# Performance work log

Measured on AMD Instinct MI355X. Metric: run time of the kernel, lower is better.

Reference implementation:

```python
import jax, jax.numpy as jnp
import numpy as np

N = 30000      # nodes
E = 300000     # edges (before self-loops)
F_NODE = 32; F_EDGE = 16
HID = 64       # hidden_channels
H = 4; C = 64  # heads, per-head channels (GATConv out_channels = HID)
NEG_SLOPE_ATT = 0.2   # GATConv negative_slope
NEG_SLOPE_ACT = 0.01  # F.leaky_relu default
LN_EPS = 1e-5


def setup_inputs() -> dict:
    key = jax.random.key(0)
    ks = jax.random.split(key, 32)
    def w(k, shape, fan_in):
        return jax.random.normal(k, shape, jnp.float32) * (1.0 / np.sqrt(fan_in))
    inp = {
        "x": jax.random.normal(ks[0], (N, F_NODE), jnp.float32),
        "edge_index": jax.random.randint(ks[1], (2, E), 0, N),
        "edge_attr": jax.random.normal(ks[2], (E, F_EDGE), jnp.float32),
        "wn": w(ks[3], (F_NODE, HID), F_NODE), "bn": jnp.zeros((HID,), jnp.float32),
        "we": w(ks[4], (F_EDGE, HID), F_EDGE), "be": jnp.zeros((HID,), jnp.float32),
    }
    for i, off in ((1, 5), (2, 13)):
        inp[f"lin{i}"] = w(ks[off], (HID, H * C), HID)        # GATConv.lin
        inp[f"line{i}"] = w(ks[off + 1], (HID, H * C), HID)    # GATConv.lin_edge
        inp[f"as{i}"] = w(ks[off + 2], (H, C), C)              # att_src
        inp[f"ad{i}"] = w(ks[off + 3], (H, C), C)              # att_dst
        inp[f"ae{i}"] = w(ks[off + 4], (H, C), C)              # att_edge
        inp[f"b{i}"] = jnp.zeros((C,), jnp.float32)            # GATConv bias (concat=False -> C)
        inp[f"g{i}"] = jnp.ones((HID,), jnp.float32)           # LayerNorm weight
        inp[f"bt{i}"] = jnp.zeros((HID,), jnp.float32)         # LayerNorm bias
    return inp


def layernorm(x, g, b):
    mu = x.mean(-1, keepdims=True)
    v = ((x - mu) ** 2).mean(-1, keepdims=True)
    return (x - mu) / jnp.sqrt(v + LN_EPS) * g + b


def gat_layer(x, src, dst, e_attr, lin_w, lin_e_w, att_src, att_dst, att_edge, bias, n):
    # x: [n, HID]; e_attr: [E2, HID]; edge lists already include self-loops
    E2 = src.shape[0]
    h = (x @ lin_w).reshape(n, H, C)          # [n,H,C]
    e = (e_attr @ lin_e_w).reshape(E2, H, C)  # [E2,H,C]
    a_src = (h * att_src[None]).sum(-1)       # [n,H]
    a_dst = (h * att_dst[None]).sum(-1)       # [n,H]
    a_edge = (e * att_edge[None]).sum(-1)     # [E2,H]
    a = jax.nn.leaky_relu(a_src[src] + a_dst[dst] + a_edge, NEG_SLOPE_ATT)
    # scatter-softmax over destination neighborhoods (every node has a self-loop)
    m = jax.ops.segment_max(a, dst, num_segments=n)
    ex = jnp.exp(a - m[dst])
    den = jax.ops.segment_sum(ex, dst, num_segments=n)
    alpha = ex / den[dst]                     # [E2,H]
    out = jax.ops.segment_sum(h[src] * alpha[..., None], dst, num_segments=n)  # [n,H,C]
    return out.mean(axis=1) + bias, alpha     # concat=False: average heads


def reference(x, edge_index, edge_attr, wn, bn, we, be,
              lin1, line1, as1, ad1, ae1, b1, g1, bt1,
              lin2, line2, as2, ad2, ae2, b2, g2, bt2):
    n = x.shape[0]
    x = jax.nn.relu(x @ wn + bn)
    ea = jax.nn.relu(edge_attr @ we + be)
    src, dst = edge_index[0], edge_index[1]
    # PyG add_self_loops(fill_value='mean'): self-loop edge_attr = mean of incoming edge_attr
    ones = jnp.ones((src.shape[0],), ea.dtype)
    deg = jax.ops.segment_sum(ones, dst, num_segments=n)
    mean_ea = jax.ops.segment_sum(ea, dst, num_segments=n) / jnp.maximum(deg, 1.0)[:, None]
    loop = jnp.arange(n, dtype=src.dtype)
    src_f = jnp.concatenate([src, loop])
    dst_f = jnp.concatenate([dst, loop])
    ea_f = jnp.concatenate([ea, mean_ea], axis=0)
    h1, alpha1 = gat_layer(x, src_f, dst_f, ea_f, lin1, line1, as1, ad1, ae1, b1, n)
    h1 = layernorm(jax.nn.leaky_relu(h1, NEG_SLOPE_ACT), g1, bt1)
    # dropout is identity in eval mode
    h2, alpha2 = gat_layer(h1, src_f, dst_f, ea_f, lin2, line2, as2, ad2, ae2, b2, n)
    h2 = layernorm(jax.nn.leaky_relu(h2, NEG_SLOPE_ACT), g2, bt2)
    return h2, alpha1, alpha2
```

## Files before the change

### kernel.cpp

```cpp
#include <hip/hip_runtime.h>

#define FN 32
#define FE 16
#define HID 64
#define HEADS 4
#define CHC 64

__device__ __forceinline__ float bf2f(unsigned short u) {
  unsigned int x = ((unsigned int)u) << 16;
  return __builtin_bit_cast(float, x);
}
__device__ __forceinline__ unsigned short f2bf(float f) {
  unsigned int x = __builtin_bit_cast(unsigned int, f);
  unsigned int r = (x + 0x7fff + ((x >> 16) & 1)) >> 16;
  return (unsigned short)r;
}

__device__ __forceinline__ void reduce8_store(const float p[8],
    float* __restrict__ arr1, float* __restrict__ arr2, size_t pos, int lane)
{
  float q[4];
  {
    bool hi = lane & 1;
    #pragma unroll
    for (int m = 0; m < 4; m++) {
      float keep = hi ? p[m + 4] : p[m];
      float send = hi ? p[m] : p[m + 4];
      q[m] = keep + __shfl_xor(send, 1);
    }
  }
  float r[2];
  {
    bool hi = lane & 2;
    #pragma unroll
    for (int m = 0; m < 2; m++) {
      float keep = hi ? q[m + 2] : q[m];
      float send = hi ? q[m] : q[m + 2];
      r[m] = keep + __shfl_xor(send, 2);
    }
  }
  float s;
  {
    bool hi = lane & 4;
    float keep = hi ? r[1] : r[0];
    float send = hi ? r[0] : r[1];
    s = keep + __shfl_xor(send, 4);
  }
  s += __shfl_xor(s, 8);
  s += __shfl_xor(s, 16);
  s += __shfl_xor(s, 32);
  if (lane < 8) {
    int entry = ((lane & 1) << 2) | (lane & 2) | ((lane >> 2) & 1);
    if (entry < 4) arr1[pos * 4 + entry] = s;
    else           arr2[pos * 4 + entry - 4] = s;
  }
}

__global__ __launch_bounds__(256) void k_vecs(
    const float* __restrict__ lin1, const float* __restrict__ line1,
    const float* __restrict__ as1, const float* __restrict__ ad1,
    const float* __restrict__ ae1,
    const float* __restrict__ lin2, const float* __restrict__ line2,
    const float* __restrict__ as2, const float* __restrict__ ad2,
    const float* __restrict__ ae2,
    float* __restrict__ vS, float* __restrict__ vD, float* __restrict__ vE)
{
  int bi = blockIdx.x;
  int l = bi / 3, kind = bi % 3;
  const float* lin = (kind == 2) ? (l ? line2 : line1) : (l ? lin2 : lin1);
  const float* att = (kind == 0) ? (l ? as2 : as1)
                   : (kind == 1) ? (l ? ad2 : ad1) : (l ? ae2 : ae1);
  float* out = ((kind == 0) ? vS : (kind == 1) ? vD : vE) + l * 256;
  int t = threadIdx.x;
  int c = t >> 2, hd = t & 3;
  float acc = 0.f;
  for (int cc = 0; cc < CHC; cc++)
    acc += lin[c * (HEADS * CHC) + hd * CHC + cc] * att[hd * CHC + cc];
  out[c * 4 + hd] = acc;
}

__global__ __launch_bounds__(256) void k_x1(const float* __restrict__ x,
    const float* __restrict__ wn, const float* __restrict__ bn,
    const float* __restrict__ vS, const float* __restrict__ vD,
    float* __restrict__ x1, float* __restrict__ ssrc, float* __restrict__ sdst,
    int n)
{
  int t = threadIdx.x; int w = t >> 6; int lane = t & 63;
  int v = blockIdx.x * 4 + w;
  __shared__ float xs[4][FN];
  if (v < n && lane < FN) xs[w][lane] = x[(size_t)v * FN + lane];
  __syncthreads();
  if (v >= n) return;
  float acc = bn[lane];
  #pragma unroll
  for (int k = 0; k < FN; k++) acc += xs[w][k] * wn[k * HID + lane];
  acc = fmaxf(acc, 0.f);
  x1[(size_t)v * HID + lane] = acc;
  float4 s4 = ((const float4*)vS)[lane];
  float4 d4 = ((const float4*)vD)[lane];
  float p[8] = {acc * s4.x, acc * s4.y, acc * s4.z, acc * s4.w,
                acc * d4.x, acc * d4.y, acc * d4.z, acc * d4.w};
  reduce8_store(p, ssrc, sdst, (size_t)v, lane);
}

__global__ __launch_bounds__(256) void k_sdots(const float* __restrict__ xin,
    const float* __restrict__ vS, const float* __restrict__ vD,
    float* __restrict__ ssrc, float* __restrict__ sdst, int n)
{
  int t = threadIdx.x; int w = t >> 6; int lane = t & 63;
  int v = blockIdx.x * 4 + w;
  if (v >= n) return;
  float xc = xin[(size_t)v * HID + lane];
  float4 s4 = ((const float4*)vS)[lane];
  float4 d4 = ((const float4*)vD)[lane];
  float p[8] = {xc * s4.x, xc * s4.y, xc * s4.z, xc * s4.w,
                xc * d4.x, xc * d4.y, xc * d4.z, xc * d4.w};
  reduce8_store(p, ssrc, sdst, (size_t)v, lane);
}

__global__ __launch_bounds__(256) void k_deg(const int* __restrict__ dst,
                                             int* __restrict__ deg, int E)
{
  int e = blockIdx.x * 256 + threadIdx.x;
  if (e < E) atomicAdd(&deg[dst[e]], 1);
}

__global__ __launch_bounds__(1024) void k_scan1(const int* __restrict__ deg,
    int* __restrict__ rowptr, int* __restrict__ bsum, int n)
{
  __shared__ int wsum[16];
  int t = threadIdx.x, wv = t >> 6, lane = t & 63;
  int i = blockIdx.x * 1024 + t;
  int val = (i < n) ? deg[i] : 0;
  int sc = val;
  #pragma unroll
  for (int off = 1; off < 64; off <<= 1) {
    int u = __shfl_up(sc, off);
    if (lane >= off) sc += u;
  }
  if (lane == 63) wsum[wv] = sc;
  __syncthreads();
  int woff = 0;
  #pragma unroll
  for (int k = 0; k < 16; k++) woff += (k < wv) ? wsum[k] : 0;
  if (i < n) rowptr[i] = woff + sc - val;
  if (t == 0) {
    int tot = 0;
    #pragma unroll
    for (int k = 0; k < 16; k++) tot += wsum[k];
    bsum[blockIdx.x] = tot;
  }
}

__global__ __launch_bounds__(1024) void k_scan2(const int* __restrict__ bsum,
    int* __restrict__ boff, int* __restrict__ rowptr, int nb, int n)
{
  __shared__ int wsum[16];
  int t = threadIdx.x, wv = t >> 6, lane = t & 63;
  int val = (t < nb) ? bsum[t] : 0;
  int sc = val;
  #pragma unroll
  for (int off = 1; off < 64; off <<= 1) {
    int u = __shfl_up(sc, off);
    if (lane >= off) sc += u;
  }
  if (lane == 63) wsum[wv] = sc;
  __syncthreads();
  int woff = 0;
  #pragma unroll
  for (int k = 0; k < 16; k++) woff += (k < wv) ? wsum[k] : 0;
  if (t < nb) boff[t] = woff + sc - val;
  if (t == 0) {
    int tot = 0;
    #pragma unroll
    for (int k = 0; k < 16; k++) tot += wsum[k];
    rowptr[n] = tot;
  }
}

__global__ __launch_bounds__(1024) void k_scan3(int* __restrict__ rowptr,
    const int* __restrict__ boff, int n)
{
  int i = blockIdx.x * 1024 + threadIdx.x;
  if (i < n) rowptr[i] += boff[blockIdx.x];
}

__global__ __launch_bounds__(256) void k_fill(const int* __restrict__ src,
    const int* __restrict__ dst, const int* __restrict__ rowptr,
    int* __restrict__ cnt, int* __restrict__ eid, int* __restrict__ srcs,
    int* __restrict__ perm, int E)
{
  int e = blockIdx.x * 256 + threadIdx.x;
  if (e < E) {
    int d = dst[e];
    int pos = rowptr[d] + atomicAdd(&cnt[d], 1);
    eid[pos] = e;
    srcs[pos] = src[e];
    perm[e] = pos;
  }
}

__global__ __launch_bounds__(256) void k_aeg_e(const float* __restrict__ eattr,
    const float* __restrict__ we, const float* __restrict__ be,
    const float* __restrict__ vE, const int* __restrict__ perm,
    float* __restrict__ aeg1, float* __restrict__ aeg2, int E)
{
  __shared__ float4 we_t4[HID][4];
  __shared__ float4 vE_s[2][HID];
  __shared__ float  be_s[HID];
  int t = threadIdx.x;
  for (int i = t; i < FE * HID; i += 256) {
    int k = i >> 6, c = i & 63;
    ((float*)we_t4)[c * 16 + k] = we[i];
  }
  for (int i = t; i < 512; i += 256) ((float*)vE_s)[i] = vE[i];
  if (t < HID) be_s[t] = be[t];
  __syncthreads();

  int e = blockIdx.x * 256 + t;
  if (e >= E) return;
  const float4* er = (const float4*)(eattr + (size_t)e * FE);
  float4 A = er[0], B = er[1], C4 = er[2], D = er[3];
  float ta[FE] = {A.x, A.y, A.z, A.w, B.x, B.y, B.z, B.w,
                  C4.x, C4.y, C4.z, C4.w, D.x, D.y, D.z, D.w};
  float4 acc1 = make_float4(0.f, 0.f, 0.f, 0.f);
  float4 acc2 = make_float4(0.f, 0.f, 0.f, 0.f);
  #pragma unroll 4
  for (int c = 0; c < HID; c++) {
    float4 w0 = we_t4[c][0], w1 = we_t4[c][1], w2 = we_t4[c][2], w3 = we_t4[c][3];
    float ea = be_s[c];
    ea += ta[0] * w0.x + ta[1] * w0.y + ta[2] * w0.z + ta[3] * w0.w;
    ea += ta[4] * w1.x + ta[5] * w1.y + ta[6] * w1.z + ta[7] * w1.w;
    ea += ta[8] * w2.x + ta[9] * w2.y + ta[10] * w2.z + ta[11] * w2.w;
    ea += ta[12] * w3.x + ta[13] * w3.y + ta[14] * w3.z + ta[15] * w3.w;
    ea = fmaxf(ea, 0.f);
    float4 u1 = vE_s[0][c], u2 = vE_s[1][c];
    acc1.x += ea * u1.x; acc1.y += ea * u1.y; acc1.z += ea * u1.z; acc1.w += ea * u1.w;
    acc2.x += ea * u2.x; acc2.y += ea * u2.y; acc2.z += ea * u2.z; acc2.w += ea * u2.w;
  }
  int pos = perm[e];
  *(float4*)(aeg1 + (size_t)pos * 4) = acc1;
  *(float4*)(aeg2 + (size_t)pos * 4) = acc2;
}

__global__ __launch_bounds__(256) void k_self_aeg(const int* __restrict__ rowptr,
    float* __restrict__ aeg1, float* __restrict__ aeg2, int E, int n)
{
  int t = threadIdx.x;
  int v = blockIdx.x * 32 + (t >> 3);
  if (v >= n) return;
  int ent = t & 7;
  int h = ent & 3;
  const float* srcp = (ent < 4) ? aeg1 : aeg2;
  int r0 = rowptr[v], r1 = rowptr[v + 1];
  float s = 0.f;
  for (int j = r0; j < r1; j++) s += srcp[(size_t)j * 4 + h];
  float m = s / fmaxf((float)(r1 - r0), 1.f);
  if (ent < 4) aeg1[((size_t)E + v) * 4 + h] = m;
  else         aeg2[((size_t)E + v) * 4 + h] = m;
}

#define NPB 16
__global__ __launch_bounds__(256) void k_h(const float* __restrict__ xin,
    const float* __restrict__ lin, unsigned short* __restrict__ h_bf, int n)
{
  int t = threadIdx.x;
  int v0 = blockIdx.x * NPB;
  __shared__ float xs[NPB][HID];
  for (int i = t; i < NPB * HID; i += 256) {
    int vv = v0 + (i >> 6);
    xs[i >> 6][i & 63] = (vv < n) ? xin[(size_t)vv * HID + (i & 63)] : 0.f;
  }
  __syncthreads();
  float acc[NPB];
  #pragma unroll
  for (int i = 0; i < NPB; i++) acc[i] = 0.f;
  for (int k = 0; k < HID; k++) {
    float lv = lin[k * 256 + t];
    #pragma unroll
    for (int i = 0; i < NPB; i++) acc[i] += xs[i][k] * lv;
  }
  #pragma unroll
  for (int i = 0; i < NPB; i++) {
    int v = v0 + i;
    if (v < n) h_bf[(size_t)v * 256 + t] = f2bf(acc[i]);
  }
}

__global__ __launch_bounds__(256) void k_node(
    const unsigned short* __restrict__ h_bf, const float* __restrict__ ssrc,
    const float* __restrict__ sdst, const float* __restrict__ aegc,
    const int* __restrict__ rowptr, const int* __restrict__ eidArr,
    const int* __restrict__ srcs, const float* __restrict__ bias,
    const float* __restrict__ gamma, const float* __restrict__ beta,
    float* __restrict__ alpha_out, float* __restrict__ xout, int n, int E)
{
  int t = threadIdx.x; int wv = t >> 6, lane = t & 63;
  int v = blockIdx.x * 4 + wv;
  if (v >= n) return;
  int r0 = rowptr[v], r1 = rowptr[v + 1];
  int deg = r1 - r0, ne = deg + 1;
  int j = lane >> 2, h = lane & 3;
  int coff = lane * 4;
  int hh = lane >> 4;
  float sd = sdst[v * 4 + h];
  float acc0 = 0.f, acc1 = 0.f, acc2 = 0.f, acc3 = 0.f;

  if (ne <= 16) {
    int s = v, eo = E + v;
    bool valid = (j < ne);
    if (j < deg) { s = srcs[r0 + j]; eo = eidArr[r0 + j]; }
    float a = -INFINITY;
    if (valid) {
      float ae = (j < deg) ? aegc[(size_t)(r0 + j) * 4 + h]
                           : aegc[((size_t)E + v) * 4 + h];
      a = ssrc[s * 4 + h] + sd + ae;
      a = (a > 0.f) ? a : 0.2f * a;
    }
    float m = a;
    m = fmaxf(m, __shfl_xor(m, 4));
    m = fmaxf(m, __shfl_xor(m, 8));
    m = fmaxf(m, __shfl_xor(m, 16));
    m = fmaxf(m, __shfl_xor(m, 32));
    float ex = valid ? __expf(a - m) : 0.f;
    float den = ex;
    den += __shfl_xor(den, 4);
    den += __shfl_xor(den, 8);
    den += __shfl_xor(den, 16);
    den += __shfl_xor(den, 32);
    float alpha = ex / den;
    if (valid) alpha_out[(size_t)eo * 4 + h] = alpha;
    int jj = 0;
    for (; jj + 1 < ne; jj += 2) {
      int s0 = __shfl(s, jj * 4);
      int s1 = __shfl(s, jj * 4 + 4);
      float al0 = __shfl(alpha, jj * 4 + hh);
      float al1 = __shfl(alpha, jj * 4 + 4 + hh);
      uint2 u0 = *(const uint2*)(h_bf + (size_t)s0 * 256 + coff);
      uint2 u1 = *(const uint2*)(h_bf + (size_t)s1 * 256 + coff);
      acc0 += al0 * bf2f((unsigned short)(u0.x & 0xffff))
            + al1 * bf2f((unsigned short)(u1.x & 0xffff));
      acc1 += al0 * bf2f((unsigned short)(u0.x >> 16))
            + al1 * bf2f((unsigned short)(u1.x >> 16));
      acc2 += al0 * bf2f((unsigned short)(u0.y & 0xffff))
            + al1 * bf2f((unsigned short)(u1.y & 0xffff));
      acc3 += al0 * bf2f((unsigned short)(u0.y >> 16))
            + al1 * bf2f((unsigned short)(u1.y >> 16));
    }
    if (jj < ne) {
      int s0 = __shfl(s, jj * 4);
      float al0 = __shfl(alpha, jj * 4 + hh);
      uint2 u0 = *(const uint2*)(h_bf + (size_t)s0 * 256 + coff);
      acc0 += al0 * bf2f((unsigned short)(u0.x & 0xffff));
      acc1 += al0 * bf2f((unsigned short)(u0.x >> 16));
      acc2 += al0 * bf2f((unsigned short)(u0.y & 0xffff));
      acc3 += al0 * bf2f((unsigned short)(u0.y >> 16));
    }
  } else {
    float m = -INFINITY;
    for (int jb = 0; jb < ne; jb += 16) {
      int jc = jb + j;
      if (jc < ne) {
        int s2 = (jc < deg) ? srcs[r0 + jc] : v;
        float ae = (jc < deg) ? aegc[(size_t)(r0 + jc) * 4 + h]
                              : aegc[((size_t)E + v) * 4 + h];
        float a = ssrc[s2 * 4 + h] + sd + ae;
        a = (a > 0.f) ? a : 0.2f * a;
        m = fmaxf(m, a);
      }
    }
    m = fmaxf(m, __shfl_xor(m, 4));
    m = fmaxf(m, __shfl_xor(m, 8));
    m = fmaxf(m, __shfl_xor(m, 16));
    m = fmaxf(m, __shfl_xor(m, 32));
    float den = 0.f;
    for (int jb = 0; jb < ne; jb += 16) {
      int jc = jb + j;
      if (jc < ne) {
        int s2 = (jc < deg) ? srcs[r0 + jc] : v;
        float ae = (jc < deg) ? aegc[(size_t)(r0 + jc) * 4 + h]
                              : aegc[((size_t)E + v) * 4 + h];
        float a = ssrc[s2 * 4 + h] + sd + ae;
        a = (a > 0.f) ? a : 0.2f * a;
        den += __expf(a - m);
      }
    }
    den += __shfl_xor(den, 4);
    den += __shfl_xor(den, 8);
    den += __shfl_xor(den, 16);
    den += __shfl_xor(den, 32);
    float rden = 1.f / den;
    for (int jb = 0; jb < ne; jb += 16) {
      int jc = jb + j;
      if (jc < ne) {
        int s2 = (jc < deg) ? srcs[r0 + jc] : v;
        int eo = (jc < deg) ? eidArr[r0 + jc] : E + v;
        float ae = (jc < deg) ? aegc[(size_t)(r0 + jc) * 4 + h]
                              : aegc[((size_t)E + v) * 4 + h];
        float a = ssrc[s2 * 4 + h] + sd + ae;
        a = (a > 0.f) ? a : 0.2f * a;
        alpha_out[(size_t)eo * 4 + h] = __expf(a - m) * rden;
      }
    }
    float sdh = __shfl(sd, hh);
    float mh  = __shfl(m, hh);
    float rdh = __shfl(rden, hh);
    for (int jc = 0; jc < ne; jc++) {
      int s0 = (jc < deg) ? srcs[r0 + jc] : v;
      size_t ap = (jc < deg) ? (size_t)(r0 + jc) : (size_t)E + v;
      float a = ssrc[s0 * 4 + hh] + sdh + aegc[ap * 4 + hh];
      a = (a > 0.f) ? a : 0.2f * a;
      float al = __expf(a - mh) * rdh;
      uint2 u = *(const uint2*)(h_bf + (size_t)s0 * 256 + coff);
      acc0 += al * bf2f((unsigned short)(u.x & 0xffff));
      acc1 += al * bf2f((unsigned short)(u.x >> 16));
      acc2 += al * bf2f((unsigned short)(u.y & 0xffff));
      acc3 += al * bf2f((unsigned short)(u.y >> 16));
    }
  }

  acc0 += __shfl_xor(acc0, 16); acc0 += __shfl_xor(acc0, 32);
  acc1 += __shfl_xor(acc1, 16); acc1 += __shfl_xor(acc1, 32);
  acc2 += __shfl_xor(acc2, 16); acc2 += __shfl_xor(acc2, 32);
  acc3 += __shfl_xor(acc3, 16); acc3 += __shfl_xor(acc3, 32);

  float4 b4 = ((const float4*)bias)[lane & 15];
  float v0 = acc0 * 0.25f + b4.x;
  float v1 = acc1 * 0.25f + b4.y;
  float v2 = acc2 * 0.25f + b4.z;
  float v3 = acc3 * 0.25f + b4.w;
  v0 = (v0 > 0.f) ? v0 : 0.01f * v0;
  v1 = (v1 > 0.f) ? v1 : 0.01f * v1;
  v2 = (v2 > 0.f) ? v2 : 0.01f * v2;
  v3 = (v3 > 0.f) ? v3 : 0.01f * v3;
  float mu = v0 + v1 + v2 + v3;
  mu += __shfl_xor(mu, 1); mu += __shfl_xor(mu, 2);
  mu += __shfl_xor(mu, 4); mu += __shfl_xor(mu, 8);
  mu *= (1.f / 64.f);
  float d0 = v0 - mu, d1 = v1 - mu, d2 = v2 - mu, d3 = v3 - mu;
  float var = d0 * d0 + d1 * d1 + d2 * d2 + d3 * d3;
  var += __shfl_xor(var, 1); var += __shfl_xor(var, 2);
  var += __shfl_xor(var, 4); var += __shfl_xor(var, 8);
  var *= (1.f / 64.f);
  float rstd = rsqrtf(var + 1e-5f);
  if (lane < 16) {
    float4 g4 = ((const float4*)gamma)[lane];
    float4 be4 = ((const float4*)beta)[lane];
    float4 y = make_float4(d0 * rstd * g4.x + be4.x, d1 * rstd * g4.y + be4.y,
                           d2 * rstd * g4.z + be4.z, d3 * rstd * g4.w + be4.w);
    *(float4*)(xout + (size_t)v * HID + lane * 4) = y;
  }
}

extern "C" void kernel_launch(void* const* d_in, const int* in_sizes, int n_in,
                              void* d_out, int out_size, void* d_ws, size_t ws_size,
                              hipStream_t stream)
{
  const float* x     = (const float*)d_in[0];
  const int*   eidx  = (const int*)d_in[1];
  const float* eattr = (const float*)d_in[2];
  const float* wn    = (const float*)d_in[3];
  const float* bn    = (const float*)d_in[4];
  const float* we    = (const float*)d_in[5];
  const float* be    = (const float*)d_in[6];
  const float* lin1  = (const float*)d_in[7];
  const float* line1 = (const float*)d_in[8];
  const float* as1   = (const float*)d_in[9];
  const float* ad1   = (const float*)d_in[10];
  const float* ae1   = (const float*)d_in[11];
  const float* b1    = (const float*)d_in[12];
  const float* g1    = (const float*)d_in[13];
  const float* bt1   = (const float*)d_in[14];
  const float* lin2  = (const float*)d_in[15];
  const float* line2 = (const float*)d_in[16];
  const float* as2   = (const float*)d_in[17];
  const float* ad2   = (const float*)d_in[18];
  const float* ae2   = (const float*)d_in[19];
  const float* b2    = (const float*)d_in[20];
  const float* g2    = (const float*)d_in[21];
  const float* bt2   = (const float*)d_in[22];

  int n = in_sizes[0] / FN;
  int E = in_sizes[1] / 2;
  const int* srcA = eidx;
  const int* dstA = eidx + E;

  float* out_h2 = (float*)d_out;
  float* alpha1 = out_h2 + (size_t)n * HID;
  float* alpha2 = alpha1 + (size_t)(E + n) * 4;

  char* ws = (char*)d_ws;
  size_t off = 0;
  auto alloc = [&](size_t bytes) -> char* {
    char* p = ws + off;
    off += (bytes + 255) & ~(size_t)255;
    return p;
  };
  unsigned short* h_bf = (unsigned short*)alloc((size_t)n * 256 * 2);
  float* x1      = (float*)alloc((size_t)n * HID * 4);
  float* h1      = (float*)alloc((size_t)n * HID * 4);
  float* aeg1c   = (float*)alloc((size_t)(E + n) * 4 * 4);
  float* aeg2c   = (float*)alloc((size_t)(E + n) * 4 * 4);
  float* ssrc    = (float*)alloc((size_t)n * 4 * 4);
  float* sdst    = (float*)alloc((size_t)n * 4 * 4);
  float* vS      = (float*)alloc(512 * 4);
  float* vD      = (float*)alloc(512 * 4);
  float* vE      = (float*)alloc(512 * 4);
  int*   deg     = (int*)alloc((size_t)n * 4);
  int*   cnt     = (int*)alloc((size_t)n * 4);
  int*   rowptr  = (int*)alloc((size_t)(n + 1) * 4);
  int*   eid     = (int*)alloc((size_t)E * 4);
  int*   srcs    = (int*)alloc((size_t)E * 4);
  int*   perm    = (int*)alloc((size_t)E * 4);
  int*   bsum    = (int*)alloc(1024 * 4);
  int*   boff    = (int*)alloc(1024 * 4);

  hipMemsetAsync(deg, 0, (size_t)n * 4, stream);
  hipMemsetAsync(cnt, 0, (size_t)n * 4, stream);

  int nb = (n + 1023) / 1024;
  k_vecs<<<6, 256, 0, stream>>>(lin1, line1, as1, ad1, ae1,
                                lin2, line2, as2, ad2, ae2, vS, vD, vE);
  k_x1<<<(n + 3) / 4, 256, 0, stream>>>(x, wn, bn, vS, vD, x1, ssrc, sdst, n);
  k_deg<<<(E + 255) / 256, 256, 0, stream>>>(dstA, deg, E);
  k_scan1<<<nb, 1024, 0, stream>>>(deg, rowptr, bsum, n);
  k_scan2<<<1, 1024, 0, stream>>>(bsum, boff, rowptr, nb, n);
  k_scan3<<<nb, 1024, 0, stream>>>(rowptr, boff, n);
  k_fill<<<(E + 255) / 256, 256, 0, stream>>>(srcA, dstA, rowptr, cnt, eid, srcs, perm, E);
  k_aeg_e<<<(E + 255) / 256, 256, 0, stream>>>(eattr, we, be, vE, perm, aeg1c, aeg2c, E);
  k_self_aeg<<<(n + 31) / 32, 256, 0, stream>>>(rowptr, aeg1c, aeg2c, E, n);

  k_h<<<(n + NPB - 1) / NPB, 256, 0, stream>>>(x1, lin1, h_bf, n);
  k_node<<<(n + 3) / 4, 256, 0, stream>>>(h_bf, ssrc, sdst, aeg1c, rowptr, eid, srcs,
                                          b1, g1, bt1, alpha1, h1, n, E);
  k_sdots<<<(n + 3) / 4, 256, 0, stream>>>(h1, vS + 256, vD + 256, ssrc, sdst, n);
  k_h<<<(n + NPB - 1) / NPB, 256, 0, stream>>>(h1, lin2, h_bf, n);
  k_node<<<(n + 3) / 4, 256, 0, stream>>>(h_bf, ssrc, sdst, aeg2c, rowptr, eid, srcs,
                                          b2, g2, bt2, alpha2, out_h2, n, E);
}
```

Baseline: 252.6 us.

## Fuse layer-2 attention dot products into k_node and widen its fast path

Removes the separate k_sdots kernel by computing the next layer's source/destination attention scores inside the first k_node epilogue, writing them to new double-buffered ssrc2/sdst2 arrays. The fast path now handles up to 64 edges with one edge per lane, loads all four head scores as float4, stages alphas in shared memory and unrolls the gather by four. Alpha outputs use nontemporal stores. The wider path lowers occupancy per edge lane for low-degree nodes and adds shared-memory use.

```diff
diff --git a/kernel.cpp b/kernel.cpp
--- a/kernel.cpp
+++ b/kernel.cpp
@@ -6,6 +6,8 @@
 #define HEADS 4
 #define CHC 64
 
+typedef float f32x4 __attribute__((ext_vector_type(4)));
+
 __device__ __forceinline__ float bf2f(unsigned short u) {
   unsigned int x = ((unsigned int)u) << 16;
   return __builtin_bit_cast(float, x);
@@ -17,7 +19,8 @@
 }
 
 __device__ __forceinline__ void reduce8_store(const float p[8],
-    float* __restrict__ arr1, float* __restrict__ arr2, size_t pos, int lane)
+    float* __restrict__ arr1, float* __restrict__ arr2, size_t pos, int lane,
+    float scale)
 {
   float q[4];
   {
@@ -51,8 +54,8 @@
   s += __shfl_xor(s, 32);
   if (lane < 8) {
     int entry = ((lane & 1) << 2) | (lane & 2) | ((lane >> 2) & 1);
-    if (entry < 4) arr1[pos * 4 + entry] = s;
-    else           arr2[pos * 4 + entry - 4] = s;
+    if (entry < 4) arr1[pos * 4 + entry] = s * scale;
+    else           arr2[pos * 4 + entry - 4] = s * scale;
   }
 }
 
@@ -100,22 +103,7 @@
   float4 d4 = ((const float4*)vD)[lane];
   float p[8] = {acc * s4.x, acc * s4.y, acc * s4.z, acc * s4.w,
                 acc * d4.x, acc * d4.y, acc * d4.z, acc * d4.w};
-  reduce8_store(p, ssrc, sdst, (size_t)v, lane);
-}
-
-__global__ __launch_bounds__(256) void k_sdots(const float* __restrict__ xin,
-    const float* __restrict__ vS, const float* __restrict__ vD,
-    float* __restrict__ ssrc, float* __restrict__ sdst, int n)
-{
-  int t = threadIdx.x; int w = t >> 6; int lane = t & 63;
-  int v = blockIdx.x * 4 + w;
-  if (v >= n) return;
-  float xc = xin[(size_t)v * HID + lane];
-  float4 s4 = ((const float4*)vS)[lane];
-  float4 d4 = ((const float4*)vD)[lane];
-  float p[8] = {xc * s4.x, xc * s4.y, xc * s4.z, xc * s4.w,
-                xc * d4.x, xc * d4.y, xc * d4.z, xc * d4.w};
-  reduce8_store(p, ssrc, sdst, (size_t)v, lane);
+  reduce8_store(p, ssrc, sdst, (size_t)v, lane, 1.f);
 }
 
 __global__ __launch_bounds__(256) void k_deg(const int* __restrict__ dst,
@@ -287,69 +275,115 @@
   }
 }
 
+template<bool DOTS>
 __global__ __launch_bounds__(256) void k_node(
     const unsigned short* __restrict__ h_bf, const float* __restrict__ ssrc,
     const float* __restrict__ sdst, const float* __restrict__ aegc,
     const int* __restrict__ rowptr, const int* __restrict__ eidArr,
     const int* __restrict__ srcs, const float* __restrict__ bias,
     const float* __restrict__ gamma, const float* __restrict__ beta,
-    float* __restrict__ alpha_out, float* __restrict__ xout, int n, int E)
-{
+    const float* __restrict__ vS2, const float* __restrict__ vD2,
+    float* __restrict__ alpha_out, float* __restrict__ xout,
+    float* __restrict__ ssrc_o, float* __restrict__ sdst_o, int n, int E)
+{
+  __shared__ float als[4][64][4];
   int t = threadIdx.x; int wv = t >> 6, lane = t & 63;
   int v = blockIdx.x * 4 + wv;
   if (v >= n) return;
   int r0 = rowptr[v], r1 = rowptr[v + 1];
   int deg = r1 - r0, ne = deg + 1;
-  int j = lane >> 2, h = lane & 3;
   int coff = lane * 4;
   int hh = lane >> 4;
-  float sd = sdst[v * 4 + h];
   float acc0 = 0.f, acc1 = 0.f, acc2 = 0.f, acc3 = 0.f;
-
-  if (ne <= 16) {
+  const float4* aeg4 = (const float4*)aegc;
+  const float4* ss4p = (const float4*)ssrc;
+  float4 sd4 = ((const float4*)sdst)[v];
+
+  if (ne <= 64) {
     int s = v, eo = E + v;
-    bool valid = (j < ne);
-    if (j < deg) { s = srcs[r0 + j]; eo = eidArr[r0 + j]; }
-    float a = -INFINITY;
+    if (lane < deg) { s = srcs[r0 + lane]; eo = eidArr[r0 + lane]; }
+    bool valid = (lane < ne);
+    float a0 = -INFINITY, a1 = -INFINITY, a2 = -INFINITY, a3 = -INFINITY;
     if (valid) {
-      float ae = (j < deg) ? aegc[(size_t)(r0 + j) * 4 + h]
-                           : aegc[((size_t)E + v) * 4 + h];
-      a = ssrc[s * 4 + h] + sd + ae;
-      a = (a > 0.f) ? a : 0.2f * a;
-    }
-    float m = a;
-    m = fmaxf(m, __shfl_xor(m, 4));
-    m = fmaxf(m, __shfl_xor(m, 8));
-    m = fmaxf(m, __shfl_xor(m, 16));
-    m = fmaxf(m, __shfl_xor(m, 32));
-    float ex = valid ? __expf(a - m) : 0.f;
-    float den = ex;
-    den += __shfl_xor(den, 4);
-    den += __shfl_xor(den, 8);
-    den += __shfl_xor(den, 16);
-    den += __shfl_xor(den, 32);
-    float alpha = ex / den;
-    if (valid) alpha_out[(size_t)eo * 4 + h] = alpha;
+      float4 ae4 = aeg4[(lane < deg) ? (r0 + lane) : (E + v)];
+      float4 ss4 = ss4p[s];
+      a0 = ss4.x + sd4.x + ae4.x; a0 = (a0 > 0.f) ? a0 : 0.2f * a0;
+      a1 = ss4.y + sd4.y + ae4.y; a1 = (a1 > 0.f) ? a1 : 0.2f * a1;
+      a2 = ss4.z + sd4.z + ae4.z; a2 = (a2 > 0.f) ? a2 : 0.2f * a2;
+      a3 = ss4.w + sd4.w + ae4.w; a3 = (a3 > 0.f) ? a3 : 0.2f * a3;
+    }
+    float m0, m1, m2, m3;
+    {
+      bool hi0 = lane & 1;
+      float k0 = hi0 ? a2 : a0, s0 = hi0 ? a0 : a2;
+      float k1 = hi0 ? a3 : a1, s1 = hi0 ? a1 : a3;
+      float q0 = fmaxf(k0, __shfl_xor(s0, 1));
+      float q1 = fmaxf(k1, __shfl_xor(s1, 1));
+      bool hi1 = lane & 2;
+      float k2 = hi1 ? q1 : q0, s2 = hi1 ? q0 : q1;
+      float r = fmaxf(k2, __shfl_xor(s2, 2));
+      r = fmaxf(r, __shfl_xor(r, 4));
+      r = fmaxf(r, __shfl_xor(r, 8));
+      r = fmaxf(r, __shfl_xor(r, 16));
+      r = fmaxf(r, __shfl_xor(r, 32));
+      m0 = __shfl(r, 0); m1 = __shfl(r, 2); m2 = __shfl(r, 1); m3 = __shfl(r, 3);
+    }
+    float e0 = __expf(a0 - m0), e1 = __expf(a1 - m1);
+    float e2 = __expf(a2 - m2), e3 = __expf(a3 - m3);
+    float d0, d1, d2, d3;
+    {
+      bool hi0 = lane & 1;
+      float k0 = hi0 ? e2 : e0, s0 = hi0 ? e0 : e2;
+      float k1 = hi0 ? e3 : e1, s1 = hi0 ? e1 : e3;
+      float q0 = k0 + __shfl_xor(s0, 1);
+      float q1 = k1 + __shfl_xor(s1, 1);
+      bool hi1 = lane & 2;
+      float k2 = hi1 ? q1 : q0, s2 = hi1 ? q0 : q1;
+      float r = k2 + __shfl_xor(s2, 2);
+      r += __shfl_xor(r, 4);
+      r += __shfl_xor(r, 8);
+      r += __shfl_xor(r, 16);
+      r += __shfl_xor(r, 32);
+      d0 = __shfl(r, 0); d1 = __shfl(r, 2); d2 = __shfl(r, 1); d3 = __shfl(r, 3);
+    }
+    float4 alf = make_float4(e0 / d0, e1 / d1, e2 / d2, e3 / d3);
+    if (valid) {
+      f32x4 alv = {alf.x, alf.y, alf.z, alf.w};
+      __builtin_nontemporal_store(alv, (f32x4*)alpha_out + eo);
+    }
+    *(float4*)als[wv][lane] = alf;
+    __builtin_amdgcn_wave_barrier();
+    __builtin_amdgcn_sched_barrier(0);
     int jj = 0;
-    for (; jj + 1 < ne; jj += 2) {
-      int s0 = __shfl(s, jj * 4);
-      int s1 = __shfl(s, jj * 4 + 4);
-      float al0 = __shfl(alpha, jj * 4 + hh);
-      float al1 = __shfl(alpha, jj * 4 + 4 + hh);
+    for (; jj + 3 < ne; jj += 4) {
+      int s0 = __shfl(s, jj), s1 = __shfl(s, jj + 1);
+      int s2 = __shfl(s, jj + 2), s3 = __shfl(s, jj + 3);
+      float al0 = als[wv][jj][hh],     al1 = als[wv][jj + 1][hh];
+      float al2 = als[wv][jj + 2][hh], al3 = als[wv][jj + 3][hh];
       uint2 u0 = *(const uint2*)(h_bf + (size_t)s0 * 256 + coff);
       uint2 u1 = *(const uint2*)(h_bf + (size_t)s1 * 256 + coff);
+      uint2 u2 = *(const uint2*)(h_bf + (size_t)s2 * 256 + coff);
+      uint2 u3 = *(const uint2*)(h_bf + (size_t)s3 * 256 + coff);
       acc0 += al0 * bf2f((unsigned short)(u0.x & 0xffff))
-            + al1 * bf2f((unsigned short)(u1.x & 0xffff));
+            + al1 * bf2f((unsigned short)(u1.x & 0xffff))
+            + al2 * bf2f((unsigned short)(u2.x & 0xffff))
+            + al3 * bf2f((unsigned short)(u3.x & 0xffff));
       acc1 += al0 * bf2f((unsigned short)(u0.x >> 16))
-            + al1 * bf2f((unsigned short)(u1.x >> 16));
+            + al1 * bf2f((unsigned short)(u1.x >> 16))
+            + al2 * bf2f((unsigned short)(u2.x >> 16))
+            + al3 * bf2f((unsigned short)(u3.x >> 16));
       acc2 += al0 * bf2f((unsigned short)(u0.y & 0xffff))
-            + al1 * bf2f((unsigned short)(u1.y & 0xffff));
+            + al1 * bf2f((unsigned short)(u1.y & 0xffff))
+            + al2 * bf2f((unsigned short)(u2.y & 0xffff))
+            + al3 * bf2f((unsigned short)(u3.y & 0xffff));
       acc3 += al0 * bf2f((unsigned short)(u0.y >> 16))
-            + al1 * bf2f((unsigned short)(u1.y >> 16));
-    }
-    if (jj < ne) {
-      int s0 = __shfl(s, jj * 4);
-      float al0 = __shfl(alpha, jj * 4 + hh);
+            + al1 * bf2f((unsigned short)(u1.y >> 16))
+            + al2 * bf2f((unsigned short)(u2.y >> 16))
+            + al3 * bf2f((unsigned short)(u3.y >> 16));
+    }
+    for (; jj < ne; jj++) {
+      int s0 = __shfl(s, jj);
+      float al0 = als[wv][jj][hh];
       uint2 u0 = *(const uint2*)(h_bf + (size_t)s0 * 256 + coff);
       acc0 += al0 * bf2f((unsigned short)(u0.x & 0xffff));
       acc1 += al0 * bf2f((unsigned short)(u0.x >> 16));
@@ -357,14 +391,16 @@
       acc3 += al0 * bf2f((unsigned short)(u0.y >> 16));
     }
   } else {
+    int j4 = lane >> 2, hb = lane & 3;
+    float sd = sdst[v * 4 + hb];
     float m = -INFINITY;
     for (int jb = 0; jb < ne; jb += 16) {
-      int jc = jb + j;
+      int jc = jb + j4;
       if (jc < ne) {
         int s2 = (jc < deg) ? srcs[r0 + jc] : v;
-        float ae = (jc < deg) ? aegc[(size_t)(r0 + jc) * 4 + h]
-                              : aegc[((size_t)E + v) * 4 + h];
-        float a = ssrc[s2 * 4 + h] + sd + ae;
+        float ae = (jc < deg) ? aegc[(size_t)(r0 + jc) * 4 + hb]
+                              : aegc[((size_t)E + v) * 4 + hb];
+        float a = ssrc[s2 * 4 + hb] + sd + ae;
         a = (a > 0.f) ? a : 0.2f * a;
         m = fmaxf(m, a);
       }
@@ -375,12 +411,12 @@
     m = fmaxf(m, __shfl_xor(m, 32));
     float den = 0.f;
     for (int jb = 0; jb < ne; jb += 16) {
-      int jc = jb + j;
+      int jc = jb + j4;
       if (jc < ne) {
         int s2 = (jc < deg) ? srcs[r0 + jc] : v;
-        float ae = (jc < deg) ? aegc[(size_t)(r0 + jc) * 4 + h]
-                              : aegc[((size_t)E + v) * 4 + h];
-        float a = ssrc[s2 * 4 + h] + sd + ae;
+        float ae = (jc < deg) ? aegc[(size_t)(r0 + jc) * 4 + hb]
+                              : aegc[((size_t)E + v) * 4 + hb];
+        float a = ssrc[s2 * 4 + hb] + sd + ae;
         a = (a > 0.f) ? a : 0.2f * a;
         den += __expf(a - m);
       }
@@ -391,15 +427,15 @@
     den += __shfl_xor(den, 32);
     float rden = 1.f / den;
     for (int jb = 0; jb < ne; jb += 16) {
-      int jc = jb + j;
+      int jc = jb + j4;
       if (jc < ne) {
         int s2 = (jc < deg) ? srcs[r0 + jc] : v;
         int eo = (jc < deg) ? eidArr[r0 + jc] : E + v;
-        float ae = (jc < deg) ? aegc[(size_t)(r0 + jc) * 4 + h]
-                              : aegc[((size_t)E + v) * 4 + h];
-        float a = ssrc[s2 * 4 + h] + sd + ae;
+        float ae = (jc < deg) ? aegc[(size_t)(r0 + jc) * 4 + hb]
+                              : aegc[((size_t)E + v) * 4 + hb];
+        float a = ssrc[s2 * 4 + hb] + sd + ae;
         a = (a > 0.f) ? a : 0.2f * a;
-        alpha_out[(size_t)eo * 4 + h] = __expf(a - m) * rden;
+        alpha_out[(size_t)eo * 4 + hb] = __expf(a - m) * rden;
       }
     }
     float sdh = __shfl(sd, hh);
@@ -424,7 +460,8 @@
   acc2 += __shfl_xor(acc2, 16); acc2 += __shfl_xor(acc2, 32);
   acc3 += __shfl_xor(acc3, 16); acc3 += __shfl_xor(acc3, 32);
 
-  float4 b4 = ((const float4*)bias)[lane & 15];
+  int c16 = lane & 15;
+  float4 b4 = ((const float4*)bias)[c16];
   float v0 = acc0 * 0.25f + b4.x;
   float v1 = acc1 * 0.25f + b4.y;
   float v2 = acc2 * 0.25f + b4.z;
@@ -443,12 +480,32 @@
   var += __shfl_xor(var, 4); var += __shfl_xor(var, 8);
   var *= (1.f / 64.f);
   float rstd = rsqrtf(var + 1e-5f);
+  float4 g4 = ((const float4*)gamma)[c16];
+  float4 be4 = ((const float4*)beta)[c16];
+  float y0 = d0 * rstd * g4.x + be4.x;
+  float y1 = d1 * rstd * g4.y + be4.y;
+  float y2 = d2 * rstd * g4.z + be4.z;
+  float y3 = d3 * rstd * g4.w + be4.w;
   if (lane < 16) {
-    float4 g4 = ((const float4*)gamma)[lane];
-    float4 be4 = ((const float4*)beta)[lane];
-    float4 y = make_float4(d0 * rstd * g4.x + be4.x, d1 * rstd * g4.y + be4.y,
-                           d2 * rstd * g4.z + be4.z, d3 * rstd * g4.w + be4.w);
+    float4 y = make_float4(y0, y1, y2, y3);
     *(float4*)(xout + (size_t)v * HID + lane * 4) = y;
+  }
+  if constexpr (DOTS) {
+    int c0 = c16 * 4;
+    float4 vs0 = ((const float4*)vS2)[c0],     vs1 = ((const float4*)vS2)[c0 + 1];
+    float4 vs2 = ((const float4*)vS2)[c0 + 2], vs3 = ((const float4*)vS2)[c0 + 3];
+    float4 vd0 = ((const float4*)vD2)[c0],     vd1 = ((const float4*)vD2)[c0 + 1];
+    float4 vd2 = ((const float4*)vD2)[c0 + 2], vd3 = ((const float4*)vD2)[c0 + 3];
+    float p[8];
+    p[0] = y0 * vs0.x + y1 * vs1.x + y2 * vs2.x + y3 * vs3.x;
+    p[1] = y0 * vs0.y + y1 * vs1.y + y2 * vs2.y + y3 * vs3.y;
+    p[2] = y0 * vs0.z + y1 * vs1.z + y2 * vs2.z + y3 * vs3.z;
+    p[3] = y0 * vs0.w + y1 * vs1.w + y2 * vs2.w + y3 * vs3.w;
+    p[4] = y0 * vd0.x + y1 * vd1.x + y2 * vd2.x + y3 * vd3.x;
+    p[5] = y0 * vd0.y + y1 * vd1.y + y2 * vd2.y + y3 * vd3.y;
+    p[6] = y0 * vd0.z + y1 * vd1.z + y2 * vd2.z + y3 * vd3.z;
+    p[7] = y0 * vd0.w + y1 * vd1.w + y2 * vd2.w + y3 * vd3.w;
+    reduce8_store(p, ssrc_o, sdst_o, (size_t)v, lane, 0.25f);
   }
 }
 
@@ -501,8 +558,10 @@
   float* h1      = (float*)alloc((size_t)n * HID * 4);
   float* aeg1c   = (float*)alloc((size_t)(E + n) * 4 * 4);
   float* aeg2c   = (float*)alloc((size_t)(E + n) * 4 * 4);
-  float* ssrc    = (float*)alloc((size_t)n * 4 * 4);
-  float* sdst    = (float*)alloc((size_t)n * 4 * 4);
+  float* ssrc1   = (float*)alloc((size_t)n * 4 * 4);
+  float* sdst1   = (float*)alloc((size_t)n * 4 * 4);
+  float* ssrc2   = (float*)alloc((size_t)n * 4 * 4);
+  float* sdst2   = (float*)alloc((size_t)n * 4 * 4);
   float* vS      = (float*)alloc(512 * 4);
   float* vD      = (float*)alloc(512 * 4);
   float* vE      = (float*)alloc(512 * 4);
@@ -521,7 +580,7 @@
   int nb = (n + 1023) / 1024;
   k_vecs<<<6, 256, 0, stream>>>(lin1, line1, as1, ad1, ae1,
                                 lin2, line2, as2, ad2, ae2, vS, vD, vE);
-  k_x1<<<(n + 3) / 4, 256, 0, stream>>>(x, wn, bn, vS, vD, x1, ssrc, sdst, n);
+  k_x1<<<(n + 3) / 4, 256, 0, stream>>>(x, wn, bn, vS, vD, x1, ssrc1, sdst1, n);
   k_deg<<<(E + 255) / 256, 256, 0, stream>>>(dstA, deg, E);
   k_scan1<<<nb, 1024, 0, stream>>>(deg, rowptr, bsum, n);
   k_scan2<<<1, 1024, 0, stream>>>(bsum, boff, rowptr, nb, n);
@@ -531,10 +590,11 @@
   k_self_aeg<<<(n + 31) / 32, 256, 0, stream>>>(rowptr, aeg1c, aeg2c, E, n);
 
   k_h<<<(n + NPB - 1) / NPB, 256, 0, stream>>>(x1, lin1, h_bf, n);
-  k_node<<<(n + 3) / 4, 256, 0, stream>>>(h_bf, ssrc, sdst, aeg1c, rowptr, eid, srcs,
-                                          b1, g1, bt1, alpha1, h1, n, E);
-  k_sdots<<<(n + 3) / 4, 256, 0, stream>>>(h1, vS + 256, vD + 256, ssrc, sdst, n);
+  k_node<true><<<(n + 3) / 4, 256, 0, stream>>>(h_bf, ssrc1, sdst1, aeg1c,
+      rowptr, eid, srcs, b1, g1, bt1, vS + 256, vD + 256,
+      alpha1, h1, ssrc2, sdst2, n, E);
   k_h<<<(n + NPB - 1) / NPB, 256, 0, stream>>>(h1, lin2, h_bf, n);
-  k_node<<<(n + 3) / 4, 256, 0, stream>>>(h_bf, ssrc, sdst, aeg2c, rowptr, eid, srcs,
-                                          b2, g2, bt2, alpha2, out_h2, n, E);
-}
+  k_node<false><<<(n + 3) / 4, 256, 0, stream>>>(h_bf, ssrc2, sdst2, aeg2c,
+      rowptr, eid, srcs, b2, g2, bt2, nullptr, nullptr,
+      alpha2, out_h2, nullptr, nullptr, n, E);
+}
```

After: 228.2 us. 1.11x faster.
